# Kernel optimization log

Hardware: AMD Instinct MI355X
Metric: run time of the kernel (lower is better)

The kernel has to match this reference:

```python
import jax, jax.numpy as jnp
import numpy as np
import math

H = 16
D_MODEL = 1024
D_K = D_MODEL // H
B = 4
S = 2048


def setup_inputs() -> dict:
    key = jax.random.key(0)
    ks = jax.random.split(key, 11)
    s_in = 1.0 / math.sqrt(D_MODEL)
    inp = {
        "query": jax.random.normal(ks[0], (B, S, D_MODEL), dtype=jnp.float32),
        "key_": jax.random.normal(ks[1], (B, S, D_MODEL), dtype=jnp.float32),
        "value": jax.random.normal(ks[2], (B, S, D_MODEL), dtype=jnp.float32),
        # stacked per-head projection weights: [h, d_model, d_k]
        "Wq": jax.random.uniform(ks[3], (H, D_MODEL, D_K), jnp.float32, -s_in, s_in),
        "bq": jax.random.uniform(ks[4], (H, D_K), jnp.float32, -s_in, s_in),
        "Wk": jax.random.uniform(ks[5], (H, D_MODEL, D_K), jnp.float32, -s_in, s_in),
        "bk": jax.random.uniform(ks[6], (H, D_K), jnp.float32, -s_in, s_in),
        "Wv": jax.random.uniform(ks[7], (H, D_MODEL, D_K), jnp.float32, -s_in, s_in),
        "bv": jax.random.uniform(ks[8], (H, D_K), jnp.float32, -s_in, s_in),
        "Wo": jax.random.uniform(ks[9], (D_MODEL, D_MODEL), jnp.float32, -s_in, s_in),
        "bo": jax.random.uniform(ks[10], (D_MODEL,), jnp.float32, -s_in, s_in),
    }
    return inp


def reference(query, key_, value, Wq, bq, Wk, bk, Wv, bv, Wo, bo):
    # Per-head projections, batched over heads: [b,s,m] x [h,m,k] -> [b,h,s,k]
    q = jnp.einsum("bsm,hmk->bhsk", query, Wq) + bq[None, :, None, :]
    k = jnp.einsum("bsm,hmk->bhsk", key_, Wk) + bk[None, :, None, :]
    v = jnp.einsum("bsm,hmk->bhsk", value, Wv) + bv[None, :, None, :]
    # scores: q @ k^T -> [b,h,Sq,Sk]
    scores = jnp.einsum("bhqk,bhsk->bhqs", q, k) / jnp.sqrt(jnp.float32(D_K))
    # NOTE: original code softmaxes over dim=1 of the per-head [N,Sq,Sk]
    # tensor, i.e. the QUERY axis (axis=2 here). Mask has no effect
    # (masked_fill result is discarded in the source), so it is omitted.
    attn = jax.nn.softmax(scores, axis=2)
    ctx = jnp.einsum("bhqs,bhsk->bhqk", attn, v)  # [b,h,Sq,d_k]
    # concat heads along last dim (head-major order matches torch.cat)
    ctx = jnp.transpose(ctx, (0, 2, 1, 3)).reshape(B, S, D_MODEL)
    out = ctx @ Wo.T + bo  # final_W; dropout = identity (eval mode)
    return out
```

## Files before the change

### kernel.cpp

```cpp
#include <hip/hip_runtime.h>


#define DEV __device__ __forceinline__

typedef __bf16 bf16x8 __attribute__((ext_vector_type(8)));
typedef float  f32x4  __attribute__((ext_vector_type(4)));

DEV unsigned short f2bf(float f) {
    __bf16 h = (__bf16)f;
    return __builtin_bit_cast(unsigned short, h);
}

DEV bf16x8 ldfrag(const unsigned short* p) {
    return *reinterpret_cast<const bf16x8*>(p);
}

DEV float fast_exp2(float x) {
#if __has_builtin(__builtin_amdgcn_exp2f)
    return __builtin_amdgcn_exp2f(x);
#else
    return exp2f(x);
#endif
}

DEV void gld16(const unsigned short* g, unsigned short* l) {
    __builtin_amdgcn_global_load_lds(
        (__attribute__((address_space(1))) void*)g,
        (__attribute__((address_space(3))) void*)l, 16, 0, 0);
}

#define MFMA(a,b,c) __builtin_amdgcn_mfma_f32_16x16x32_bf16((a),(b),(c),0,0,0)

#define QSCALE 0.18033688011112042f

__global__ __launch_bounds__(256) void wprep(const float* __restrict__ Wq,
                                             const float* __restrict__ Wk,
                                             const float* __restrict__ Wv,
                                             const float* __restrict__ Wo,
                                             unsigned short* __restrict__ Wt,
                                             unsigned short* __restrict__ Wot) {
    int idx = blockIdx.x * 256 + threadIdx.x;
    int which = blockIdx.y;
    if (which == 3) { Wot[idx] = f2bf(Wo[idx]); return; }
    const float* W = (which == 0) ? Wq : (which == 1) ? Wk : Wv;
    int n = idx >> 10, m = idx & 1023;
    int h = n >> 6, k = n & 63;
    Wt[(size_t)which * 1048576 + idx] = f2bf(W[h * 65536 + m * 64 + k]);
}

__global__ __launch_bounds__(256) void xprep(const float* __restrict__ X,
                                             unsigned short* __restrict__ Xb) {
    int idx = (blockIdx.x * 256 + threadIdx.x) * 4;
    float4 f = *(const float4*)&X[idx];
    ushort4 o;
    o.x = f2bf(f.x); o.y = f2bf(f.y); o.z = f2bf(f.z); o.w = f2bf(f.w);
    *(ushort4*)&Xb[idx] = o;
}

__global__ __launch_bounds__(256) void proj_gemm(
        const unsigned short* __restrict__ Xb, const unsigned short* __restrict__ Bt,
        const float* __restrict__ bias, unsigned short* __restrict__ O,
        unsigned short* __restrict__ Vt, int z) {
    const int tid = threadIdx.x;
    const int bm = blockIdx.x, bn = blockIdx.y;

    __shared__ __align__(16) unsigned short As[128 * 32];
    __shared__ __align__(16) unsigned short Bs[128 * 32];

    const int lane = tid & 63, wid = tid >> 6;
    const int l16 = lane & 15, quad = lane >> 4;
    const int wm = wid & 1, wn = wid >> 1;

    const unsigned short* ga =
        Xb + (size_t)(bm * 128 + wid * 32 + (lane >> 2)) * 1024 + (lane & 3) * 8;
    const unsigned short* gb =
        Bt + (size_t)(bn * 128 + wid * 32 + (lane >> 2)) * 1024 + (lane & 3) * 8;
    unsigned short* la = &As[wid * 32 * 32];
    unsigned short* lb = &Bs[wid * 32 * 32];

    f32x4 acc[4][4] = {};
    for (int kt = 0; kt < 32; ++kt) {
        __syncthreads();
        const int k0 = kt * 32;
        gld16(ga + k0, la);
        gld16(ga + k0 + 16 * 1024, la + 16 * 32);
        gld16(gb + k0, lb);
        gld16(gb + k0 + 16 * 1024, lb + 16 * 32);
        __syncthreads();
        bf16x8 af[4], bfr[4];
#pragma unroll
        for (int mi = 0; mi < 4; ++mi)
            af[mi] = ldfrag(&As[(wm * 64 + mi * 16 + l16) * 32 + quad * 8]);
#pragma unroll
        for (int ni = 0; ni < 4; ++ni)
            bfr[ni] = ldfrag(&Bs[(wn * 64 + ni * 16 + l16) * 32 + quad * 8]);
#pragma unroll
        for (int mi = 0; mi < 4; ++mi)
#pragma unroll
            for (int ni = 0; ni < 4; ++ni)
                acc[mi][ni] = MFMA(af[mi], bfr[ni], acc[mi][ni]);
    }

#pragma unroll
    for (int mi = 0; mi < 4; ++mi)
#pragma unroll
        for (int ni = 0; ni < 4; ++ni)
#pragma unroll
            for (int r = 0; r < 4; ++r) {
                int row = bm * 128 + wm * 64 + mi * 16 + quad * 4 + r;
                int col = bn * 128 + wn * 64 + ni * 16 + l16;
                float v = acc[mi][ni][r] + bias[col];
                if (z == 0) v *= QSCALE;
                int b = row >> 11, s = row & 2047;
                int h = col >> 6, k = col & 63;
                unsigned short o = f2bf(v);
                if (z == 2) {
                    Vt[(size_t)((b * 16 + h) * 64 + k) * 2048 + s] = o;
                } else {
                    O[(size_t)((b * 16 + h) * 2048 + s) * 64 + k] = o;
                }
            }
}

__global__ __launch_bounds__(256) void colsum_vscale(
        const unsigned short* __restrict__ Qh, const unsigned short* __restrict__ Kh,
        unsigned short* __restrict__ Vt) {
    const int tid = threadIdx.x;
    const int st = blockIdx.x, bh = blockIdx.y;
    const unsigned short* Qb = Qh + (size_t)bh * 2048 * 64;
    const unsigned short* Kb = Kh + (size_t)bh * 2048 * 64;

    __shared__ __align__(16) unsigned short Qs[2][128 * 64];
    __shared__ float Dtmp[2][128];
    __shared__ float Dsh[128];

    const int lane = tid & 63, wid = tid >> 6;
    const int l16 = lane & 15, quad = lane >> 4;
    const int wm = wid & 1, wn = wid >> 1;
    const int l7 = l16 & 7;

    bf16x8 kf[2][4];
#pragma unroll
    for (int ks = 0; ks < 2; ++ks)
#pragma unroll
        for (int ni = 0; ni < 4; ++ni)
            kf[ks][ni] = ldfrag(&Kb[(size_t)(st * 128 + wn * 64 + ni * 16 + l16) * 64 +
                                    ks * 32 + quad * 8]);

    const unsigned short* gq = Qb + (size_t)(wid * 32 + (lane >> 3)) * 64 +
                               ((lane & 7) ^ (lane >> 3)) * 8;

#pragma unroll
    for (int gi = 0; gi < 4; ++gi)
        gld16(gq + (size_t)gi * 8 * 64, &Qs[0][(wid * 32 + gi * 8) * 64]);

    float psum[4] = {0.f, 0.f, 0.f, 0.f};
    for (int it = 0; it < 16; ++it) {
        const int buf = it & 1;
        __syncthreads();
        if (it < 15) {
            const size_t q1 = (size_t)(it + 1) * 128;
#pragma unroll
            for (int gi = 0; gi < 4; ++gi)
                gld16(gq + (q1 + gi * 8) * 64, &Qs[buf ^ 1][(wid * 32 + gi * 8) * 64]);
        }
        f32x4 acc[4][4] = {};
#pragma unroll
        for (int ks = 0; ks < 2; ++ks) {
            bf16x8 af[4];
#pragma unroll
            for (int mi = 0; mi < 4; ++mi)
                af[mi] = ldfrag(&Qs[buf][(wm * 64 + mi * 16 + l16) * 64 +
                                         (((ks * 4 + quad) ^ l7) * 8)]);
#pragma unroll
            for (int mi = 0; mi < 4; ++mi)
#pragma unroll
                for (int ni = 0; ni < 4; ++ni)
                    acc[mi][ni] = MFMA(af[mi], kf[ks][ni], acc[mi][ni]);
        }
#pragma unroll
        for (int ni = 0; ni < 4; ++ni) {
            float d = 0.f;
#pragma unroll
            for (int mi = 0; mi < 4; ++mi)
#pragma unroll
                for (int r = 0; r < 4; ++r)
                    d += fast_exp2(acc[mi][ni][r]);
            psum[ni] += d;
        }
    }
#pragma unroll
    for (int ni = 0; ni < 4; ++ni) {
        float v = psum[ni];
        v += __shfl_xor(v, 16, 64);
        v += __shfl_xor(v, 32, 64);
        if (quad == 0) Dtmp[wm][wn * 64 + ni * 16 + l16] = v;
    }
    __syncthreads();
    if (tid < 128) Dsh[tid] = 1.0f / (Dtmp[0][tid] + Dtmp[1][tid]);
    __syncthreads();

    const int k = tid >> 2, c = tid & 3;
    unsigned short* vrow = Vt + ((size_t)bh * 64 + k) * 2048 + st * 128 + c * 32;
#pragma unroll
    for (int j = 0; j < 4; ++j) {
        bf16x8 v = *(const bf16x8*)&vrow[j * 8];
        bf16x8 o;
#pragma unroll
        for (int e = 0; e < 8; ++e)
            o[e] = (__bf16)((float)v[e] * Dsh[c * 32 + j * 8 + e]);
        *(bf16x8*)&vrow[j * 8] = o;
    }
}

__global__ __launch_bounds__(256) void attnpv(const unsigned short* __restrict__ Qh,
                                              const unsigned short* __restrict__ Kh,
                                              const unsigned short* __restrict__ Vn,
                                              unsigned short* __restrict__ Ctx) {
    const int tid = threadIdx.x;
    const int qt = blockIdx.x, bh = blockIdx.y;
    const int b = bh >> 4, h = bh & 15;
    const unsigned short* Qb = Qh + (size_t)bh * 2048 * 64;
    const unsigned short* Kb = Kh + (size_t)bh * 2048 * 64;
    const unsigned short* Vb = Vn + (size_t)bh * 64 * 2048;

    __shared__ __align__(16) unsigned char smem[49152];
    unsigned short* Ks = (unsigned short*)smem;
    unsigned short* Vs = (unsigned short*)(smem + 16384);
    unsigned short* Pw = (unsigned short*)(smem + 32768) + (tid >> 6) * 2048;

    const int lane = tid & 63, wid = tid >> 6;
    const int l16 = lane & 15, quad = lane >> 4;
    const int wq = wid & 1, ws = wid >> 1;
    const int l7 = l16 & 7;
    const int ph = (l16 >> 1) & 7;
    const int pql = l16 & 1;

    bf16x8 qf[2][4];
#pragma unroll
    for (int ks = 0; ks < 2; ++ks)
#pragma unroll
        for (int nj = 0; nj < 4; ++nj)
            qf[ks][nj] = ldfrag(&Qb[(size_t)(qt * 128 + wq * 64 + nj * 16 + l16) * 64 +
                                    ks * 32 + quad * 8]);

    const int half = wid & 1;
    const int sr8 = lane >> 3;
    const int sg = ((lane & 7) ^ sr8) * 8;
    const unsigned short* gk = Kb + (size_t)(half * 32 + sr8) * 64 + sg;
    const unsigned short* gv = Vb + (size_t)(half * 32 + sr8) * 2048 + sg;

    if (wid < 2) {
#pragma unroll
        for (int gi = 0; gi < 4; ++gi)
            gld16(gk + (size_t)gi * 8 * 64, &Ks[(half * 32 + gi * 8) * 64]);
    } else {
#pragma unroll
        for (int gi = 0; gi < 4; ++gi)
            gld16(gv + (size_t)gi * 8 * 2048, &Vs[(half * 32 + gi * 8) * 64]);
    }

    f32x4 cacc[4][4] = {};
    for (int it = 0; it < 32; ++it) {
        const int pb = it & 1;
        __syncthreads();

        if (it < 31) {
            const size_t s1 = (size_t)(it + 1) * 64;
            if (wid < 2) {
#pragma unroll
                for (int gi = 0; gi < 4; ++gi)
                    gld16(gk + (s1 + gi * 8) * 64,
                          &Ks[(pb ^ 1) * 4096 + (half * 32 + gi * 8) * 64]);
            } else {
#pragma unroll
                for (int gi = 0; gi < 4; ++gi)
                    gld16(gv + (size_t)gi * 8 * 2048 + s1,
                          &Vs[(pb ^ 1) * 4096 + (half * 32 + gi * 8) * 64]);
            }
        }

        bf16x8 kf[2][2];
#pragma unroll
        for (int mi = 0; mi < 2; ++mi)
#pragma unroll
            for (int ks = 0; ks < 2; ++ks)
                kf[mi][ks] = ldfrag(&Ks[pb * 4096 + (ws * 32 + mi * 16 + l16) * 64 +
                                        (((ks * 4 + quad) ^ l7) * 8)]);
        f32x4 sacc[2][4] = {};
#pragma unroll
        for (int ks = 0; ks < 2; ++ks)
#pragma unroll
            for (int mi = 0; mi < 2; ++mi)
#pragma unroll
                for (int nj = 0; nj < 4; ++nj)
                    sacc[mi][nj] = MFMA(kf[mi][ks], qf[ks][nj], sacc[mi][nj]);

#pragma unroll
        for (int mi = 0; mi < 2; ++mi) {
            const int G = pql * 4 + mi * 2 + (quad >> 1);
            const int po = ((G ^ ph) * 8) + (quad & 1) * 4;
#pragma unroll
            for (int nj = 0; nj < 4; ++nj) {
                ushort4 p;
                p.x = f2bf(fast_exp2(sacc[mi][nj][0]));
                p.y = f2bf(fast_exp2(sacc[mi][nj][1]));
                p.z = f2bf(fast_exp2(sacc[mi][nj][2]));
                p.w = f2bf(fast_exp2(sacc[mi][nj][3]));
                *(ushort4*)&Pw[(nj * 8 + (l16 >> 1)) * 64 + po] = p;
            }
        }

        bf16x8 vf[4], pf[4];
#pragma unroll
        for (int mi = 0; mi < 4; ++mi)
            vf[mi] = ldfrag(&Vs[pb * 4096 + (mi * 16 + l16) * 64 +
                                (((ws * 4 + quad) ^ l7) * 8)]);
#pragma unroll
        for (int nj = 0; nj < 4; ++nj)
            pf[nj] = ldfrag(&Pw[(nj * 8 + (l16 >> 1)) * 64 +
                                (((pql * 4 + quad) ^ ph) * 8)]);
#pragma unroll
        for (int mi = 0; mi < 4; ++mi)
#pragma unroll
            for (int nj = 0; nj < 4; ++nj)
                cacc[mi][nj] = MFMA(vf[mi], pf[nj], cacc[mi][nj]);
    }

    __syncthreads();
    f32x4* Red = (f32x4*)smem;
    if (ws == 1) {
#pragma unroll
        for (int mi = 0; mi < 4; ++mi)
#pragma unroll
            for (int nj = 0; nj < 4; ++nj)
                Red[(wq * 16 + mi * 4 + nj) * 64 + lane] = cacc[mi][nj];
    }
    __syncthreads();
    if (ws == 0) {
#pragma unroll
        for (int mi = 0; mi < 4; ++mi)
#pragma unroll
            for (int nj = 0; nj < 4; ++nj) {
                f32x4 t = Red[(wq * 16 + mi * 4 + nj) * 64 + lane];
                int q = qt * 128 + wq * 64 + nj * 16 + l16;
                int k = mi * 16 + quad * 4;
                ushort4 o;
                o.x = f2bf(cacc[mi][nj][0] + t[0]);
                o.y = f2bf(cacc[mi][nj][1] + t[1]);
                o.z = f2bf(cacc[mi][nj][2] + t[2]);
                o.w = f2bf(cacc[mi][nj][3] + t[3]);
                *(ushort4*)&Ctx[(size_t)(b * 2048 + q) * 1024 + h * 64 + k] = o;
            }
    }
}

__global__ __launch_bounds__(256) void out_gemm(const unsigned short* __restrict__ A,
                                                const unsigned short* __restrict__ Bt,
                                                const float* __restrict__ bias,
                                                float* __restrict__ Out) {
    const int tid = threadIdx.x;
    const int bm = blockIdx.x, bn = blockIdx.y;

    __shared__ __align__(16) unsigned short As[128 * 32];
    __shared__ __align__(16) unsigned short Bs[128 * 32];

    const int lane = tid & 63, wid = tid >> 6;
    const int l16 = lane & 15, quad = lane >> 4;
    const int wm = wid & 1, wn = wid >> 1;

    const unsigned short* ga =
        A + (size_t)(bm * 128 + wid * 32 + (lane >> 2)) * 1024 + (lane & 3) * 8;
    const unsigned short* gb =
        Bt + (size_t)(bn * 128 + wid * 32 + (lane >> 2)) * 1024 + (lane & 3) * 8;
    unsigned short* la = &As[wid * 32 * 32];
    unsigned short* lb = &Bs[wid * 32 * 32];

    f32x4 acc[4][4] = {};
    for (int kt = 0; kt < 32; ++kt) {
        __syncthreads();
        const int k0 = kt * 32;
        gld16(ga + k0, la);
        gld16(ga + k0 + 16 * 1024, la + 16 * 32);
        gld16(gb + k0, lb);
        gld16(gb + k0 + 16 * 1024, lb + 16 * 32);
        __syncthreads();
        bf16x8 af[4], bfr[4];
#pragma unroll
        for (int mi = 0; mi < 4; ++mi)
            af[mi] = ldfrag(&As[(wm * 64 + mi * 16 + l16) * 32 + quad * 8]);
#pragma unroll
        for (int ni = 0; ni < 4; ++ni)
            bfr[ni] = ldfrag(&Bs[(wn * 64 + ni * 16 + l16) * 32 + quad * 8]);
#pragma unroll
        for (int mi = 0; mi < 4; ++mi)
#pragma unroll
            for (int ni = 0; ni < 4; ++ni)
                acc[mi][ni] = MFMA(af[mi], bfr[ni], acc[mi][ni]);
    }
#pragma unroll
    for (int mi = 0; mi < 4; ++mi)
#pragma unroll
        for (int ni = 0; ni < 4; ++ni)
#pragma unroll
            for (int r = 0; r < 4; ++r) {
                int row = bm * 128 + wm * 64 + mi * 16 + quad * 4 + r;
                int col = bn * 128 + wn * 64 + ni * 16 + l16;
                Out[(size_t)row * 1024 + col] = acc[mi][ni][r] + bias[col];
            }
}

extern "C" void kernel_launch(void* const* d_in, const int* in_sizes, int n_in,
                              void* d_out, int out_size, void* d_ws, size_t ws_size,
                              hipStream_t stream) {
    (void)in_sizes; (void)n_in; (void)out_size; (void)ws_size;
    const float* X[3] = {(const float*)d_in[0], (const float*)d_in[1],
                         (const float*)d_in[2]};
    const float* Wq = (const float*)d_in[3];
    const float* bq = (const float*)d_in[4];
    const float* Wk = (const float*)d_in[5];
    const float* bk = (const float*)d_in[6];
    const float* Wv = (const float*)d_in[7];
    const float* bv = (const float*)d_in[8];
    const float* Wo = (const float*)d_in[9];
    const float* bo = (const float*)d_in[10];
    const float* bias[3] = {bq, bk, bv};
    float* Out = (float*)d_out;

    char* ws = (char*)d_ws;
    const size_t MB = 1024 * 1024;
    unsigned short* Wt  = (unsigned short*)(ws);
    unsigned short* Wot = (unsigned short*)(ws + 6 * MB);
    unsigned short* Qh  = (unsigned short*)(ws + 8 * MB);
    unsigned short* Kh  = (unsigned short*)(ws + 24 * MB);
    unsigned short* Vt  = (unsigned short*)(ws + 40 * MB);
    unsigned short* Ctx = (unsigned short*)(ws + 56 * MB);
    unsigned short* Xb  = Ctx;
    unsigned short* Oz[3] = {Qh, Kh, Qh };

    wprep<<<dim3(4096, 4), dim3(256), 0, stream>>>(Wq, Wk, Wv, Wo, Wt, Wot);
    for (int z = 0; z < 3; ++z) {
        xprep<<<dim3(8192), dim3(256), 0, stream>>>(X[z], Xb);
        proj_gemm<<<dim3(64, 8), dim3(256), 0, stream>>>(
            Xb, Wt + (size_t)z * 1048576, bias[z], Oz[z], Vt, z);
    }
    colsum_vscale<<<dim3(16, 64), dim3(256), 0, stream>>>(Qh, Kh, Vt);
    attnpv<<<dim3(16, 64), dim3(256), 0, stream>>>(Qh, Kh, Vt, Ctx);
    out_gemm<<<dim3(64, 8), dim3(256), 0, stream>>>(Ctx, Wot, bo, Out);
}
```

Before: 429.1 us.

## Load Q/K/V MFMA fragments directly from global memory, dropping LDS staging

In colsum_vscale and attnpv, the double-buffered LDS staging of Q, K and V tiles (with per-iteration __syncthreads) is removed. Each wave now loads its MFMA fragments straight from global memory into registers, relying on L1/L2 caching for reuse across waves. s_setprio is also raised around MFMA blocks to favor matrix issue. This removes barrier and LDS traffic but duplicates global loads across waves and exposes global latency without explicit prefetch.

```diff
diff --git a/kernel.cpp b/kernel.cpp
--- a/kernel.cpp
+++ b/kernel.cpp
@@ -130,14 +130,12 @@
     const unsigned short* Qb = Qh + (size_t)bh * 2048 * 64;
     const unsigned short* Kb = Kh + (size_t)bh * 2048 * 64;
 
-    __shared__ __align__(16) unsigned short Qs[2][128 * 64];
     __shared__ float Dtmp[2][128];
     __shared__ float Dsh[128];
 
     const int lane = tid & 63, wid = tid >> 6;
     const int l16 = lane & 15, quad = lane >> 4;
     const int wm = wid & 1, wn = wid >> 1;
-    const int l7 = l16 & 7;
 
     bf16x8 kf[2][4];
 #pragma unroll
@@ -147,36 +145,25 @@
             kf[ks][ni] = ldfrag(&Kb[(size_t)(st * 128 + wn * 64 + ni * 16 + l16) * 64 +
                                     ks * 32 + quad * 8]);
 
-    const unsigned short* gq = Qb + (size_t)(wid * 32 + (lane >> 3)) * 64 +
-                               ((lane & 7) ^ (lane >> 3)) * 8;
-
-#pragma unroll
-    for (int gi = 0; gi < 4; ++gi)
-        gld16(gq + (size_t)gi * 8 * 64, &Qs[0][(wid * 32 + gi * 8) * 64]);
+    const unsigned short* abase = Qb + (size_t)(wm * 64 + l16) * 64 + quad * 8;
 
     float psum[4] = {0.f, 0.f, 0.f, 0.f};
     for (int it = 0; it < 16; ++it) {
-        const int buf = it & 1;
-        __syncthreads();
-        if (it < 15) {
-            const size_t q1 = (size_t)(it + 1) * 128;
-#pragma unroll
-            for (int gi = 0; gi < 4; ++gi)
-                gld16(gq + (q1 + gi * 8) * 64, &Qs[buf ^ 1][(wid * 32 + gi * 8) * 64]);
-        }
+        const size_t q0 = (size_t)it * 128;
         f32x4 acc[4][4] = {};
 #pragma unroll
         for (int ks = 0; ks < 2; ++ks) {
             bf16x8 af[4];
 #pragma unroll
             for (int mi = 0; mi < 4; ++mi)
-                af[mi] = ldfrag(&Qs[buf][(wm * 64 + mi * 16 + l16) * 64 +
-                                         (((ks * 4 + quad) ^ l7) * 8)]);
+                af[mi] = ldfrag(abase + (q0 + mi * 16) * 64 + ks * 32);
+            __builtin_amdgcn_s_setprio(1);
 #pragma unroll
             for (int mi = 0; mi < 4; ++mi)
 #pragma unroll
                 for (int ni = 0; ni < 4; ++ni)
                     acc[mi][ni] = MFMA(af[mi], kf[ks][ni], acc[mi][ni]);
+            __builtin_amdgcn_s_setprio(0);
         }
 #pragma unroll
         for (int ni = 0; ni < 4; ++ni) {
@@ -224,15 +211,12 @@
     const unsigned short* Kb = Kh + (size_t)bh * 2048 * 64;
     const unsigned short* Vb = Vn + (size_t)bh * 64 * 2048;
 
-    __shared__ __align__(16) unsigned char smem[49152];
-    unsigned short* Ks = (unsigned short*)smem;
-    unsigned short* Vs = (unsigned short*)(smem + 16384);
-    unsigned short* Pw = (unsigned short*)(smem + 32768) + (tid >> 6) * 2048;
+    __shared__ __align__(16) unsigned char smem[32768];
+    unsigned short* Pw = (unsigned short*)smem + (tid >> 6) * 2048;
 
     const int lane = tid & 63, wid = tid >> 6;
     const int l16 = lane & 15, quad = lane >> 4;
     const int wq = wid & 1, ws = wid >> 1;
-    const int l7 = l16 & 7;
     const int ph = (l16 >> 1) & 7;
     const int pql = l16 & 1;
 
@@ -244,50 +228,26 @@
             qf[ks][nj] = ldfrag(&Qb[(size_t)(qt * 128 + wq * 64 + nj * 16 + l16) * 64 +
                                     ks * 32 + quad * 8]);
 
-    const int half = wid & 1;
-    const int sr8 = lane >> 3;
-    const int sg = ((lane & 7) ^ sr8) * 8;
-    const unsigned short* gk = Kb + (size_t)(half * 32 + sr8) * 64 + sg;
-    const unsigned short* gv = Vb + (size_t)(half * 32 + sr8) * 2048 + sg;
-
-    if (wid < 2) {
-#pragma unroll
-        for (int gi = 0; gi < 4; ++gi)
-            gld16(gk + (size_t)gi * 8 * 64, &Ks[(half * 32 + gi * 8) * 64]);
-    } else {
-#pragma unroll
-        for (int gi = 0; gi < 4; ++gi)
-            gld16(gv + (size_t)gi * 8 * 2048, &Vs[(half * 32 + gi * 8) * 64]);
-    }
+    const unsigned short* kbase = Kb + (size_t)(ws * 32 + l16) * 64 + quad * 8;
+    const unsigned short* vbase = Vb + (size_t)l16 * 2048 + ws * 32 + quad * 8;
 
     f32x4 cacc[4][4] = {};
     for (int it = 0; it < 32; ++it) {
-        const int pb = it & 1;
-        __syncthreads();
-
-        if (it < 31) {
-            const size_t s1 = (size_t)(it + 1) * 64;
-            if (wid < 2) {
-#pragma unroll
-                for (int gi = 0; gi < 4; ++gi)
-                    gld16(gk + (s1 + gi * 8) * 64,
-                          &Ks[(pb ^ 1) * 4096 + (half * 32 + gi * 8) * 64]);
-            } else {
-#pragma unroll
-                for (int gi = 0; gi < 4; ++gi)
-                    gld16(gv + (size_t)gi * 8 * 2048 + s1,
-                          &Vs[(pb ^ 1) * 4096 + (half * 32 + gi * 8) * 64]);
-            }
-        }
+        const size_t s0 = (size_t)it * 64;
 
         bf16x8 kf[2][2];
 #pragma unroll
         for (int mi = 0; mi < 2; ++mi)
 #pragma unroll
             for (int ks = 0; ks < 2; ++ks)
-                kf[mi][ks] = ldfrag(&Ks[pb * 4096 + (ws * 32 + mi * 16 + l16) * 64 +
-                                        (((ks * 4 + quad) ^ l7) * 8)]);
+                kf[mi][ks] = ldfrag(kbase + (s0 + mi * 16) * 64 + ks * 32);
+        bf16x8 vf[4];
+#pragma unroll
+        for (int mi = 0; mi < 4; ++mi)
+            vf[mi] = ldfrag(vbase + (size_t)(mi * 16) * 2048 + s0);
+
         f32x4 sacc[2][4] = {};
+        __builtin_amdgcn_s_setprio(1);
 #pragma unroll
         for (int ks = 0; ks < 2; ++ks)
 #pragma unroll
@@ -295,6 +255,7 @@
 #pragma unroll
                 for (int nj = 0; nj < 4; ++nj)
                     sacc[mi][nj] = MFMA(kf[mi][ks], qf[ks][nj], sacc[mi][nj]);
+        __builtin_amdgcn_s_setprio(0);
 
 #pragma unroll
         for (int mi = 0; mi < 2; ++mi) {
@@ -311,20 +272,18 @@
             }
         }
 
-        bf16x8 vf[4], pf[4];
-#pragma unroll
-        for (int mi = 0; mi < 4; ++mi)
-            vf[mi] = ldfrag(&Vs[pb * 4096 + (mi * 16 + l16) * 64 +
-                                (((ws * 4 + quad) ^ l7) * 8)]);
+        bf16x8 pf[4];
 #pragma unroll
         for (int nj = 0; nj < 4; ++nj)
             pf[nj] = ldfrag(&Pw[(nj * 8 + (l16 >> 1)) * 64 +
                                 (((pql * 4 + quad) ^ ph) * 8)]);
+        __builtin_amdgcn_s_setprio(1);
 #pragma unroll
         for (int mi = 0; mi < 4; ++mi)
 #pragma unroll
             for (int nj = 0; nj < 4; ++nj)
                 cacc[mi][nj] = MFMA(vf[mi], pf[nj], cacc[mi][nj]);
+        __builtin_amdgcn_s_setprio(0);
     }
 
     __syncthreads();
```

Measured after the change: 494.6 us. +15.3%, slower.

## Build P fragments in registers via permlane swaps instead of LDS round-trip

Applied to the files above, without the earlier changes.

The attention PV kernel no longer writes exponentiated scores to a per-wave LDS buffer and reads them back as MFMA B-operands. It packs bf16 pairs and reorders them across lanes with permlane32/permlane16 swaps, falling back to shuffles when those builtins are missing. This removes 16 KB of LDS per block and the LDS write/read traffic. The launch bounds now request 4 blocks per CU, which can raise occupancy but may constrain registers or cause spills.

```diff
diff --git a/kernel.cpp b/kernel.cpp
--- a/kernel.cpp
+++ b/kernel.cpp
@@ -32,6 +32,31 @@
 #define MFMA(a,b,c) __builtin_amdgcn_mfma_f32_16x16x32_bf16((a),(b),(c),0,0,0)
 
 #define QSCALE 0.18033688011112042f
+
+DEV bf16x8 pshuffle(unsigned w00, unsigned w01, unsigned w10, unsigned w11) {
+#if __has_builtin(__builtin_amdgcn_permlane32_swap) && __has_builtin(__builtin_amdgcn_permlane16_swap)
+    auto r0 = __builtin_amdgcn_permlane32_swap((int)w00, (int)w10, false, false);
+    auto r1 = __builtin_amdgcn_permlane32_swap((int)w01, (int)w11, false, false);
+    auto s0 = __builtin_amdgcn_permlane16_swap(r0[0], r0[1], false, false);
+    auto s1 = __builtin_amdgcn_permlane16_swap(r1[0], r1[1], false, false);
+    union { int u[4]; bf16x8 v; } o;
+    o.u[0] = s0[0]; o.u[1] = s1[0]; o.u[2] = s0[1]; o.u[3] = s1[1];
+    return o.v;
+#else
+    const int lane = threadIdx.x & 63;
+    const int l16 = lane & 15, quad = lane >> 4;
+    const int sA = (quad & 1) * 32 + l16;
+    const int sB = sA + 16;
+    const bool hi = (quad >> 1) != 0;
+    unsigned a0 = hi ? (unsigned)__shfl((int)w10, sA, 64) : (unsigned)__shfl((int)w00, sA, 64);
+    unsigned a1 = hi ? (unsigned)__shfl((int)w11, sA, 64) : (unsigned)__shfl((int)w01, sA, 64);
+    unsigned b0 = hi ? (unsigned)__shfl((int)w10, sB, 64) : (unsigned)__shfl((int)w00, sB, 64);
+    unsigned b1 = hi ? (unsigned)__shfl((int)w11, sB, 64) : (unsigned)__shfl((int)w01, sB, 64);
+    union { unsigned u[4]; bf16x8 v; } o;
+    o.u[0] = a0; o.u[1] = a1; o.u[2] = b0; o.u[3] = b1;
+    return o.v;
+#endif
+}
 
 __global__ __launch_bounds__(256) void wprep(const float* __restrict__ Wq,
                                              const float* __restrict__ Wk,
@@ -213,10 +238,10 @@
     }
 }
 
-__global__ __launch_bounds__(256) void attnpv(const unsigned short* __restrict__ Qh,
-                                              const unsigned short* __restrict__ Kh,
-                                              const unsigned short* __restrict__ Vn,
-                                              unsigned short* __restrict__ Ctx) {
+__global__ __launch_bounds__(256, 4) void attnpv(const unsigned short* __restrict__ Qh,
+                                                 const unsigned short* __restrict__ Kh,
+                                                 const unsigned short* __restrict__ Vn,
+                                                 unsigned short* __restrict__ Ctx) {
     const int tid = threadIdx.x;
     const int qt = blockIdx.x, bh = blockIdx.y;
     const int b = bh >> 4, h = bh & 15;
@@ -224,17 +249,14 @@
     const unsigned short* Kb = Kh + (size_t)bh * 2048 * 64;
     const unsigned short* Vb = Vn + (size_t)bh * 64 * 2048;
 
-    __shared__ __align__(16) unsigned char smem[49152];
+    __shared__ __align__(16) unsigned char smem[32768];
     unsigned short* Ks = (unsigned short*)smem;
     unsigned short* Vs = (unsigned short*)(smem + 16384);
-    unsigned short* Pw = (unsigned short*)(smem + 32768) + (tid >> 6) * 2048;
 
     const int lane = tid & 63, wid = tid >> 6;
     const int l16 = lane & 15, quad = lane >> 4;
     const int wq = wid & 1, ws = wid >> 1;
     const int l7 = l16 & 7;
-    const int ph = (l16 >> 1) & 7;
-    const int pql = l16 & 1;
 
     bf16x8 qf[2][4];
 #pragma unroll
@@ -296,35 +318,26 @@
                 for (int nj = 0; nj < 4; ++nj)
                     sacc[mi][nj] = MFMA(kf[mi][ks], qf[ks][nj], sacc[mi][nj]);
 
-#pragma unroll
-        for (int mi = 0; mi < 2; ++mi) {
-            const int G = pql * 4 + mi * 2 + (quad >> 1);
-            const int po = ((G ^ ph) * 8) + (quad & 1) * 4;
-#pragma unroll
-            for (int nj = 0; nj < 4; ++nj) {
-                ushort4 p;
-                p.x = f2bf(fast_exp2(sacc[mi][nj][0]));
-                p.y = f2bf(fast_exp2(sacc[mi][nj][1]));
-                p.z = f2bf(fast_exp2(sacc[mi][nj][2]));
-                p.w = f2bf(fast_exp2(sacc[mi][nj][3]));
-                *(ushort4*)&Pw[(nj * 8 + (l16 >> 1)) * 64 + po] = p;
-            }
-        }
-
-        bf16x8 vf[4], pf[4];
+        bf16x8 vf[4];
 #pragma unroll
         for (int mi = 0; mi < 4; ++mi)
             vf[mi] = ldfrag(&Vs[pb * 4096 + (mi * 16 + l16) * 64 +
                                 (((ws * 4 + quad) ^ l7) * 8)]);
-#pragma unroll
-        for (int nj = 0; nj < 4; ++nj)
-            pf[nj] = ldfrag(&Pw[(nj * 8 + (l16 >> 1)) * 64 +
-                                (((pql * 4 + quad) ^ ph) * 8)]);
-#pragma unroll
-        for (int mi = 0; mi < 4; ++mi)
-#pragma unroll
-            for (int nj = 0; nj < 4; ++nj)
-                cacc[mi][nj] = MFMA(vf[mi], pf[nj], cacc[mi][nj]);
+
+#pragma unroll
+        for (int nj = 0; nj < 4; ++nj) {
+            unsigned w[2][2];
+#pragma unroll
+            for (int mi = 0; mi < 2; ++mi)
+#pragma unroll
+                for (int p = 0; p < 2; ++p)
+                    w[mi][p] = (unsigned)f2bf(fast_exp2(sacc[mi][nj][2 * p])) |
+                               ((unsigned)f2bf(fast_exp2(sacc[mi][nj][2 * p + 1])) << 16);
+            bf16x8 pf = pshuffle(w[0][0], w[0][1], w[1][0], w[1][1]);
+#pragma unroll
+            for (int mi = 0; mi < 4; ++mi)
+                cacc[mi][nj] = MFMA(vf[mi], pf, cacc[mi][nj]);
+        }
     }
 
     __syncthreads();
```

Result: slower. 778.3 us (+81.4%).
